# Kernel optimization log

Hardware: AMD Instinct MI355X
Metric: run time of the kernel (lower is better)

The kernel has to match this reference:

```python
import jax, jax.numpy as jnp
import numpy as np

N_NODES = 100000
N_EDGES = 1600000
N_LAYERS = 3
DIM = 128


def setup_inputs() -> dict:
    key = jax.random.key(0)
    k1, k2, k3, k4 = jax.random.split(key, 4)
    x = jax.random.normal(k1, (N_NODES, DIM), dtype=jnp.float32)
    edge_indices = jax.random.randint(k2, (N_LAYERS, 2, N_EDGES), 0, N_NODES, dtype=jnp.int64)
    # GCNConv weight (glorot-ish scale) and bias per layer; all layers are DIM->DIM
    W = jax.random.normal(k3, (N_LAYERS, DIM, DIM), dtype=jnp.float32) * (1.0 / np.sqrt(DIM))
    b = jax.random.normal(k4, (N_LAYERS, DIM), dtype=jnp.float32) * 0.01
    return {"x": x, "edge_indices": edge_indices, "W": W, "b": b}


def _gcn_layer(x, edge_index, W_l, b_l):
    # Module does vstack((ei[1], ei[0])) then flow='target_to_source', which is
    # equivalent to standard GCNConv (source_to_target) on the original edge_index.
    N = x.shape[0]
    loop = jnp.arange(N, dtype=edge_index.dtype)  # self loops (add_self_loops=True)
    row = jnp.concatenate([edge_index[0], loop])  # message sources
    col = jnp.concatenate([edge_index[1], loop])  # aggregation targets
    ones = jnp.ones(row.shape[0], dtype=x.dtype)
    deg = jax.ops.segment_sum(ones, col, num_segments=N)  # in-degree incl. self loop
    dis = jax.lax.rsqrt(jnp.maximum(deg, 1.0))  # deg >= 1 due to self loops
    norm = dis[row] * dis[col]  # [E+N]
    h = x @ W_l  # linear (no bias inside GCNConv's lin)
    agg = jax.ops.segment_sum(h[row] * norm[:, None], col, num_segments=N)
    return agg + b_l


def reference(x, edge_indices, W, b):
    # eval mode: dropout(p=0.5) between layers is identity
    for l in range(edge_indices.shape[0]):
        x = jax.nn.relu(_gcn_layer(x, edge_indices[l], W[l], b[l]))
    return x
```

## Files before the change

kernel.cpp:

```cpp
#include <hip/hip_runtime.h>

#define DIM 128
#define NB_MAX 512
#define CAP_B 4608
#define TILE_EDGES 4096

typedef int idx_t;

typedef __bf16 bf16x8 __attribute__((ext_vector_type(8)));
typedef float f32x4 __attribute__((ext_vector_type(4)));

static __device__ __forceinline__ unsigned int f2bf(float f) {
    unsigned int u = __float_as_uint(f);
    return (u + 0x7fffu + ((u >> 16) & 1u)) >> 16;
}
static __device__ __forceinline__ float bf2f(unsigned int hi) {
    return __uint_as_float(hi << 16);
}

__global__ void k_zero_i(int* __restrict__ p, int n) {
    int i = blockIdx.x * blockDim.x + threadIdx.x;
    if (i < n) p[i] = 0;
}

__global__ __launch_bounds__(256) void k_partition3(const idx_t* __restrict__ edges,
                                                    int* __restrict__ gcur_all,
                                                    unsigned int* __restrict__ pairs_all,
                                                    int E, int NB) {
    const int l = blockIdx.y;
    const idx_t* row = edges + (size_t)l * 2 * E;
    const idx_t* col = row + E;
    int* gcur = gcur_all + l * NB_MAX;
    unsigned int* pairs = pairs_all + (size_t)l * NB * CAP_B;

    __shared__ int s_cnt[NB_MAX];
    __shared__ int s_base[NB_MAX];
    const int tid = threadIdx.x;
    const int base_e = blockIdx.x * TILE_EDGES;

    for (int b = tid; b < NB; b += 256) s_cnt[b] = 0;
    __syncthreads();

    #pragma unroll
    for (int i = 0; i < TILE_EDGES / 256; ++i) {
        int e = base_e + tid + i * 256;
        if (e < E) atomicAdd(&s_cnt[col[e] >> 8], 1);
    }
    __syncthreads();

    for (int b = tid; b < NB; b += 256) {
        int c = s_cnt[b];
        s_base[b] = c ? atomicAdd(&gcur[b], c) : 0;
        s_cnt[b] = 0;
    }
    __syncthreads();

    #pragma unroll
    for (int i = 0; i < TILE_EDGES / 256; ++i) {
        int e = base_e + tid + i * 256;
        if (e < E) {
            int c = col[e];
            int b = c >> 8;
            int p = s_base[b] + atomicAdd(&s_cnt[b], 1);
            if (p < CAP_B)
                pairs[(size_t)b * CAP_B + p] =
                    ((unsigned int)row[e] << 8) | (unsigned int)(c & 255);
        }
    }
}

__global__ __launch_bounds__(256) void k_local_sort3(const unsigned int* __restrict__ pairs_all,
                                                     const int* __restrict__ gcur_all,
                                                     int* __restrict__ srow_all,
                                                     int* __restrict__ offs_all,
                                                     int* __restrict__ ends_all,
                                                     float* __restrict__ dis_all,
                                                     int NB, int N) {
    const int l = blockIdx.y;
    const unsigned int* pairs = pairs_all + (size_t)l * NB * CAP_B;
    const int* gcur = gcur_all + l * NB_MAX;
    int* srow = srow_all + (size_t)l * NB * CAP_B;
    int* offs = offs_all + (size_t)l * N;
    int* ends = ends_all + (size_t)l * N;
    float* dis = dis_all + (size_t)l * N;

    __shared__ int hist[256];
    __shared__ int loffs_s[256];
    __shared__ int lcur[256];
    __shared__ int rows_s[CAP_B];
    const int tid = threadIdx.x;
    const int b = blockIdx.x;
    const int lo = b * CAP_B;
    int n = gcur[b];
    if (n > CAP_B) n = CAP_B;
    const int node0 = b << 8;

    hist[tid] = 0;
    __syncthreads();
    for (int i = tid; i < n; i += 256)
        atomicAdd(&hist[pairs[lo + i] & 255u], 1);
    __syncthreads();

    int v = hist[tid];
    loffs_s[tid] = v;
    __syncthreads();
    for (int off = 1; off < 256; off <<= 1) {
        int t = (tid >= off) ? loffs_s[tid - off] : 0;
        __syncthreads();
        loffs_s[tid] += t;
        __syncthreads();
    }
    int excl = loffs_s[tid] - v;
    loffs_s[tid] = excl;
    lcur[tid] = 0;
    int node = node0 + tid;
    if (node < N) {
        offs[node] = lo + excl;
        ends[node] = lo + excl + v;
        dis[node] = rsqrtf((float)(v + 1));
    }
    __syncthreads();

    for (int i = tid; i < n; i += 256) {
        unsigned int pk = pairs[lo + i];
        int c = pk & 255u;
        int p = loffs_s[c] + atomicAdd(&lcur[c], 1);
        rows_s[p] = (int)(pk >> 8);
    }
    __syncthreads();
    for (int i = tid; i < n; i += 256) srow[lo + i] = rows_s[i];
}

template <bool BF16IN>
__global__ __launch_bounds__(512) void k_gemm_mfma(const void* __restrict__ xin,
                                                   const float* __restrict__ W,
                                                   unsigned int* __restrict__ hb,
                                                   int M) {
    __shared__ alignas(16) unsigned short Ah[128 * 32];
    __shared__ alignas(16) unsigned short Al[128 * 32];

    const int tid  = threadIdx.x;
    const int lane = tid & 63;
    const int wv   = tid >> 6;
    const int col0 = wv * 16;
    const int row0 = blockIdx.x * 128;

    union U8 { unsigned short u[8]; bf16x8 v; };
    bf16x8 Bh[4], Bl[4];
    {
        const int bcol = col0 + (lane & 15);
        #pragma unroll
        for (int t = 0; t < 4; ++t) {
            U8 uh, ul;
            #pragma unroll
            for (int j = 0; j < 8; ++j) {
                int k = t * 32 + (lane >> 4) * 8 + j;
                float w = W[k * DIM + bcol];
                unsigned int hi = f2bf(w);
                uh.u[j] = (unsigned short)hi;
                ul.u[j] = (unsigned short)f2bf(w - bf2f(hi));
            }
            Bh[t] = uh.v;
            Bl[t] = ul.v;
        }
    }

    f32x4 acc[8];
    #pragma unroll
    for (int m = 0; m < 8; ++m) acc[m] = (f32x4){0.f, 0.f, 0.f, 0.f};

    const int srow_ = tid >> 2;
    const int quad  = tid & 3;
    const int gr    = row0 + srow_;
    const int sidx  = (srow_ * 32 + quad * 8) ^ ((srow_ & 7) << 3);

    for (int t = 0; t < 4; ++t) {
        if constexpr (BF16IN) {
            const unsigned int* xb = (const unsigned int*)xin;
            uint4 v = make_uint4(0, 0, 0, 0);
            if (gr < M) v = *(const uint4*)&xb[(size_t)gr * 64 + t * 16 + quad * 4];
            __syncthreads();
            *(uint4*)&Ah[sidx] = v;
            __syncthreads();
        } else {
            const float* x = (const float*)xin;
            float f[8];
            if (gr < M) {
                const float4* xp = (const float4*)&x[(size_t)gr * DIM + t * 32 + quad * 8];
                float4 v0 = xp[0], v1 = xp[1];
                f[0] = v0.x; f[1] = v0.y; f[2] = v0.z; f[3] = v0.w;
                f[4] = v1.x; f[5] = v1.y; f[6] = v1.z; f[7] = v1.w;
            } else {
                #pragma unroll
                for (int j = 0; j < 8; ++j) f[j] = 0.0f;
            }
            unsigned int ph[4], pl[4];
            #pragma unroll
            for (int j = 0; j < 4; ++j) {
                unsigned int h0 = f2bf(f[2 * j]),     l0 = f2bf(f[2 * j] - bf2f(h0));
                unsigned int h1 = f2bf(f[2 * j + 1]), l1 = f2bf(f[2 * j + 1] - bf2f(h1));
                ph[j] = h0 | (h1 << 16);
                pl[j] = l0 | (l1 << 16);
            }
            __syncthreads();
            *(uint4*)&Ah[sidx] = make_uint4(ph[0], ph[1], ph[2], ph[3]);
            *(uint4*)&Al[sidx] = make_uint4(pl[0], pl[1], pl[2], pl[3]);
            __syncthreads();
        }

        #pragma unroll
        for (int m = 0; m < 8; ++m) {
            int lrow = m * 16 + (lane & 15);
            int idx = (lrow * 32 + (lane >> 4) * 8) ^ ((lrow & 7) << 3);
            bf16x8 ah = *(const bf16x8*)&Ah[idx];
            acc[m] = __builtin_amdgcn_mfma_f32_16x16x32_bf16(ah, Bh[t], acc[m], 0, 0, 0);
            acc[m] = __builtin_amdgcn_mfma_f32_16x16x32_bf16(ah, Bl[t], acc[m], 0, 0, 0);
            if constexpr (!BF16IN) {
                bf16x8 al = *(const bf16x8*)&Al[idx];
                acc[m] = __builtin_amdgcn_mfma_f32_16x16x32_bf16(al, Bh[t], acc[m], 0, 0, 0);
            }
        }
    }

    const int lane15 = lane & 15;
    #pragma unroll
    for (int m = 0; m < 8; ++m) {
        #pragma unroll
        for (int r = 0; r < 4; ++r) {
            float v = acc[m][r];
            float vp = __shfl_xor(v, 1);
            int grow = row0 + m * 16 + (lane >> 4) * 4 + r;
            if (!(lane15 & 1) && grow < M) {
                unsigned int p = f2bf(v) | (f2bf(vp) << 16);
                hb[(size_t)grow * 64 + wv * 8 + (lane15 >> 1)] = p;
            }
        }
    }
}

template <bool OUT_BF16>
__global__ __launch_bounds__(256) void k_aggregate(const unsigned int* __restrict__ hb,
                                                   const float* __restrict__ dis,
                                                   const int* __restrict__ offs,
                                                   const int* __restrict__ ends,
                                                   const int* __restrict__ srow,
                                                   const float* __restrict__ b,
                                                   void* __restrict__ outv, int N) {
    int node = blockIdx.x * 4 + (threadIdx.x >> 6);
    if (node >= N) return;
    int lane = threadIdx.x & 63;

    float dn = dis[node];
    unsigned int hv = hb[(size_t)node * 64 + lane];
    float ax0 = __uint_as_float(hv << 16) * dn * dn;
    float ay0 = __uint_as_float(hv & 0xffff0000u) * dn * dn;
    float ax1 = 0.f, ay1 = 0.f, ax2 = 0.f, ay2 = 0.f, ax3 = 0.f, ay3 = 0.f;

    int j = offs[node];
    const int end = ends[node];

    for (; j + 8 <= end; j += 8) {
        int r0 = srow[j],     r1 = srow[j + 1], r2 = srow[j + 2], r3 = srow[j + 3];
        int r4 = srow[j + 4], r5 = srow[j + 5], r6 = srow[j + 6], r7 = srow[j + 7];
        float w0 = dis[r0] * dn, w1 = dis[r1] * dn, w2 = dis[r2] * dn, w3 = dis[r3] * dn;
        float w4 = dis[r4] * dn, w5 = dis[r5] * dn, w6 = dis[r6] * dn, w7 = dis[r7] * dn;
        unsigned int a0 = hb[(size_t)r0 * 64 + lane];
        unsigned int a1 = hb[(size_t)r1 * 64 + lane];
        unsigned int a2 = hb[(size_t)r2 * 64 + lane];
        unsigned int a3 = hb[(size_t)r3 * 64 + lane];
        unsigned int a4 = hb[(size_t)r4 * 64 + lane];
        unsigned int a5 = hb[(size_t)r5 * 64 + lane];
        unsigned int a6 = hb[(size_t)r6 * 64 + lane];
        unsigned int a7 = hb[(size_t)r7 * 64 + lane];
        ax0 += __uint_as_float(a0 << 16) * w0; ay0 += __uint_as_float(a0 & 0xffff0000u) * w0;
        ax1 += __uint_as_float(a1 << 16) * w1; ay1 += __uint_as_float(a1 & 0xffff0000u) * w1;
        ax2 += __uint_as_float(a2 << 16) * w2; ay2 += __uint_as_float(a2 & 0xffff0000u) * w2;
        ax3 += __uint_as_float(a3 << 16) * w3; ay3 += __uint_as_float(a3 & 0xffff0000u) * w3;
        ax0 += __uint_as_float(a4 << 16) * w4; ay0 += __uint_as_float(a4 & 0xffff0000u) * w4;
        ax1 += __uint_as_float(a5 << 16) * w5; ay1 += __uint_as_float(a5 & 0xffff0000u) * w5;
        ax2 += __uint_as_float(a6 << 16) * w6; ay2 += __uint_as_float(a6 & 0xffff0000u) * w6;
        ax3 += __uint_as_float(a7 << 16) * w7; ay3 += __uint_as_float(a7 & 0xffff0000u) * w7;
    }
    for (; j + 2 <= end; j += 2) {
        int r0 = srow[j], r1 = srow[j + 1];
        float w0 = dis[r0] * dn, w1 = dis[r1] * dn;
        unsigned int a0 = hb[(size_t)r0 * 64 + lane];
        unsigned int a1 = hb[(size_t)r1 * 64 + lane];
        ax0 += __uint_as_float(a0 << 16) * w0; ay0 += __uint_as_float(a0 & 0xffff0000u) * w0;
        ax1 += __uint_as_float(a1 << 16) * w1; ay1 += __uint_as_float(a1 & 0xffff0000u) * w1;
    }
    if (j < end) {
        int r = srow[j];
        float w = dis[r] * dn;
        unsigned int a = hb[(size_t)r * 64 + lane];
        ax0 += __uint_as_float(a << 16) * w; ay0 += __uint_as_float(a & 0xffff0000u) * w;
    }

    float2 bb = ((const float2*)b)[lane];
    float ox = (ax0 + ax1) + (ax2 + ax3) + bb.x;
    float oy = (ay0 + ay1) + (ay2 + ay3) + bb.y;
    ox = ox > 0.0f ? ox : 0.0f;
    oy = oy > 0.0f ? oy : 0.0f;
    if constexpr (OUT_BF16) {
        ((unsigned int*)outv)[(size_t)node * 64 + lane] = f2bf(ox) | (f2bf(oy) << 16);
    } else {
        ((float2*)outv)[(size_t)node * 64 + lane] = make_float2(ox, oy);
    }
}

extern "C" void kernel_launch(void* const* d_in, const int* in_sizes, int n_in,
                              void* d_out, int out_size, void* d_ws, size_t ws_size,
                              hipStream_t stream) {
    const float* x     = (const float*)d_in[0];
    const idx_t* edges = (const idx_t*)d_in[1];
    const float* W     = (const float*)d_in[2];
    const float* b     = (const float*)d_in[3];

    const int N = in_sizes[0] / DIM;
    const int E = in_sizes[1] / 6;
    const int NB = (N + 255) >> 8;
    const size_t PADE = (size_t)NB * CAP_B;

    char* ws = (char*)d_ws;
    auto align = [](size_t v) { return (v + 255) & ~(size_t)255; };
    size_t o = 0;
    float* dis3   = (float*)(ws + o); o = align(o + (size_t)3 * N * 4);
    int*   offs3  = (int*)(ws + o);   o = align(o + (size_t)3 * N * 4);
    int*   ends3  = (int*)(ws + o);   o = align(o + (size_t)3 * N * 4);
    int*   gcur3  = (int*)(ws + o);   o = align(o + (size_t)3 * NB_MAX * 4);
    int*   srow3  = (int*)(ws + o);   o = align(o + (size_t)3 * PADE * 4);
    unsigned int* hb   = (unsigned int*)(ws + o); o = align(o + (size_t)N * 64 * 4);
    unsigned int* bufA = (unsigned int*)(ws + o); o = align(o + (size_t)N * 64 * 4);
    unsigned int* pairs3 = hb;

    const int T = 256;
    const int gAg = (N + 3) / 4;
    const int gGemm = (N + 127) / 128;
    const int gPart = (E + TILE_EDGES - 1) / TILE_EDGES;

    k_zero_i<<<(3 * NB_MAX + T - 1) / T, T, 0, stream>>>(gcur3, 3 * NB_MAX);
    k_partition3<<<dim3(gPart, 3), T, 0, stream>>>(edges, gcur3, pairs3, E, NB);
    k_local_sort3<<<dim3(NB, 3), T, 0, stream>>>(pairs3, gcur3, srow3, offs3, ends3,
                                                 dis3, NB, N);

    k_gemm_mfma<false><<<gGemm, 512, 0, stream>>>(x, W, hb, N);
    k_aggregate<true><<<gAg, T, 0, stream>>>(hb, dis3, offs3, ends3, srow3, b, bufA, N);

    k_gemm_mfma<true><<<gGemm, 512, 0, stream>>>(bufA, W + (size_t)DIM * DIM, hb, N);
    k_aggregate<true><<<gAg, T, 0, stream>>>(hb, dis3 + N, offs3 + N, ends3 + N,
                                             srow3 + PADE, b + DIM, bufA, N);

    k_gemm_mfma<true><<<gGemm, 512, 0, stream>>>(bufA, W + (size_t)2 * DIM * DIM, hb, N);
    k_aggregate<false><<<gAg, T, 0, stream>>>(hb, dis3 + 2 * (size_t)N,
                                              offs3 + 2 * (size_t)N, ends3 + 2 * (size_t)N,
                                              srow3 + 2 * PADE, b + 2 * DIM,
                                              d_out, N);
}
```

Measured before the change: 355.0 us.

## Stage partitioned edges in shared memory for coalesced bucket writes

The edge-partition kernel now keeps each thread's bucket and packed pair in registers, so edges are read only once. It runs a block-wide prefix scan over bucket counts and stages the pairs sorted by bucket in shared memory, then writes them out in order so neighbouring threads write contiguous global addresses. Block size doubles to 512 threads. In exchange the kernel uses more shared memory (about 40KB) and needs extra barriers for the scan, which may lower occupancy.

```diff
diff --git a/kernel.cpp b/kernel.cpp
--- a/kernel.cpp
+++ b/kernel.cpp
@@ -4,6 +4,8 @@
 #define NB_MAX 512
 #define CAP_B 4608
 #define TILE_EDGES 4096
+#define PT 512
+#define EPT (TILE_EDGES / PT)
 
 typedef int idx_t;
 
@@ -23,10 +25,10 @@
     if (i < n) p[i] = 0;
 }
 
-__global__ __launch_bounds__(256) void k_partition3(const idx_t* __restrict__ edges,
-                                                    int* __restrict__ gcur_all,
-                                                    unsigned int* __restrict__ pairs_all,
-                                                    int E, int NB) {
+__global__ __launch_bounds__(PT) void k_partition3(const idx_t* __restrict__ edges,
+                                                   int* __restrict__ gcur_all,
+                                                   unsigned int* __restrict__ pairs_all,
+                                                   int E, int NB) {
     const int l = blockIdx.y;
     const idx_t* row = edges + (size_t)l * 2 * E;
     const idx_t* col = row + E;
@@ -35,37 +37,66 @@
 
     __shared__ int s_cnt[NB_MAX];
     __shared__ int s_base[NB_MAX];
+    __shared__ int s_res[NB_MAX];
+    __shared__ int s_scan[PT];
+    __shared__ unsigned int s_stage[TILE_EDGES];
+    __shared__ unsigned int s_gdst[TILE_EDGES];
+
     const int tid = threadIdx.x;
     const int base_e = blockIdx.x * TILE_EDGES;
-
-    for (int b = tid; b < NB; b += 256) s_cnt[b] = 0;
-    __syncthreads();
-
+    const int cnt_total = min(TILE_EDGES, E - base_e);
+
+    for (int b = tid; b < NB; b += PT) s_cnt[b] = 0;
+    __syncthreads();
+
+    int myb[EPT];
+    unsigned int mypk[EPT];
     #pragma unroll
-    for (int i = 0; i < TILE_EDGES / 256; ++i) {
-        int e = base_e + tid + i * 256;
-        if (e < E) atomicAdd(&s_cnt[col[e] >> 8], 1);
-    }
-    __syncthreads();
-
-    for (int b = tid; b < NB; b += 256) {
-        int c = s_cnt[b];
-        s_base[b] = c ? atomicAdd(&gcur[b], c) : 0;
-        s_cnt[b] = 0;
-    }
-    __syncthreads();
-
-    #pragma unroll
-    for (int i = 0; i < TILE_EDGES / 256; ++i) {
-        int e = base_e + tid + i * 256;
+    for (int i = 0; i < EPT; ++i) {
+        int e = base_e + tid + i * PT;
         if (e < E) {
             int c = col[e];
-            int b = c >> 8;
-            int p = s_base[b] + atomicAdd(&s_cnt[b], 1);
-            if (p < CAP_B)
-                pairs[(size_t)b * CAP_B + p] =
-                    ((unsigned int)row[e] << 8) | (unsigned int)(c & 255);
-        }
+            myb[i] = c >> 8;
+            mypk[i] = ((unsigned int)row[e] << 8) | (unsigned int)(c & 255);
+            atomicAdd(&s_cnt[myb[i]], 1);
+        } else {
+            myb[i] = -1;
+        }
+    }
+    __syncthreads();
+
+    int v = (tid < NB) ? s_cnt[tid] : 0;
+    s_scan[tid] = v;
+    __syncthreads();
+    for (int off = 1; off < PT; off <<= 1) {
+        int t = (tid >= off) ? s_scan[tid - off] : 0;
+        __syncthreads();
+        s_scan[tid] += t;
+        __syncthreads();
+    }
+    if (tid < NB) {
+        s_base[tid] = s_scan[tid] - v;
+        s_res[tid] = v ? atomicAdd(&gcur[tid], v) : 0;
+        s_cnt[tid] = 0;
+    }
+    __syncthreads();
+
+    #pragma unroll
+    for (int i = 0; i < EPT; ++i) {
+        if (myb[i] >= 0) {
+            int b = myb[i];
+            int li = atomicAdd(&s_cnt[b], 1);
+            int slot = s_base[b] + li;
+            int g = s_res[b] + li;
+            s_stage[slot] = mypk[i];
+            s_gdst[slot] = (g < CAP_B) ? (unsigned int)(b * CAP_B + g) : 0xFFFFFFFFu;
+        }
+    }
+    __syncthreads();
+
+    for (int s = tid; s < cnt_total; s += PT) {
+        unsigned int d = s_gdst[s];
+        if (d != 0xFFFFFFFFu) pairs[d] = s_stage[s];
     }
 }
 
@@ -339,7 +370,7 @@
     const int gPart = (E + TILE_EDGES - 1) / TILE_EDGES;
 
     k_zero_i<<<(3 * NB_MAX + T - 1) / T, T, 0, stream>>>(gcur3, 3 * NB_MAX);
-    k_partition3<<<dim3(gPart, 3), T, 0, stream>>>(edges, gcur3, pairs3, E, NB);
+    k_partition3<<<dim3(gPart, 3), PT, 0, stream>>>(edges, gcur3, pairs3, E, NB);
     k_local_sort3<<<dim3(NB, 3), T, 0, stream>>>(pairs3, gcur3, srow3, offs3, ends3,
                                                  dis3, NB, N);
 
```

Result: faster. 318.8 us (-10.2%).
